# Performance work log

Hardware: AMD Instinct MI355X
Metric: run time of the kernel (lower is better)

## Reference

```python
import jax, jax.numpy as jnp
import numpy as np

B, N, D_IN, D_OUT = 2, 2048, 2048, 2048
H, G = 32, 8            # num_heads, num_kv_groups
HD = D_OUT // H         # head_dim = 64
R = H // G              # group_size = 4


def _rope(x, cos, sin):
    # x: (b, h, n, hd); cos/sin: (n, hd)
    hd = x.shape[-1]
    x1, x2 = x[..., : hd // 2], x[..., hd // 2:]
    rotated = jnp.concatenate((-x2, x1), axis=-1)
    return x * cos[None, None] + rotated * sin[None, None]


def setup_inputs() -> dict:
    key = jax.random.key(0)
    ks = jax.random.split(key, 6)
    x = jax.random.normal(ks[0], (B, N, D_IN), dtype=jnp.float32)
    # standard RoPE tables over full head_dim (rotate-half convention)
    inv_freq = 1.0 / (10000.0 ** (np.arange(0, HD, 2, dtype=np.float32) / HD))
    t = np.arange(N, dtype=np.float32)
    freqs = np.outer(t, inv_freq)                      # (n, hd/2)
    emb = np.concatenate([freqs, freqs], axis=-1)      # (n, hd)
    cos = jnp.asarray(np.cos(emb), dtype=jnp.float32)
    sin = jnp.asarray(np.sin(emb), dtype=jnp.float32)
    mask = jnp.triu(jnp.ones((N, N), dtype=bool), k=1)  # True above diagonal -> masked
    s = 0.02
    Wq = jax.random.normal(ks[1], (D_IN, D_OUT), dtype=jnp.float32) * s
    Wk = jax.random.normal(ks[2], (D_IN, G * HD), dtype=jnp.float32) * s
    Wv = jax.random.normal(ks[3], (D_IN, G * HD), dtype=jnp.float32) * s
    Wo = jax.random.normal(ks[4], (D_OUT, D_OUT), dtype=jnp.float32) * s
    return {"x": x, "cos": cos, "sin": sin, "mask": mask,
            "Wq": Wq, "Wk": Wk, "Wv": Wv, "Wo": Wo}


def reference(x, cos, sin, mask, Wq, Wk, Wv, Wo):
    b, n, _ = x.shape
    q = (x @ Wq).reshape(b, n, H, HD).transpose(0, 2, 1, 3)   # (b, H, n, hd)
    k = (x @ Wk).reshape(b, n, G, HD).transpose(0, 2, 1, 3)   # (b, G, n, hd)
    v = (x @ Wv).reshape(b, n, G, HD).transpose(0, 2, 1, 3)   # (b, G, n, hd)
    q = _rope(q, cos, sin)
    k = _rope(k, cos, sin)
    # grouped attention: avoid physically repeating KV heads
    qg = q.reshape(b, G, R, n, HD)                            # (b, G, r, n, hd)
    scores = jnp.einsum('bgrnd,bgmd->bgrnm', qg, k)           # (b, G, r, n, n)
    scores = jnp.where(mask[None, None, None], -jnp.inf, scores)
    attn = jax.nn.softmax(scores / jnp.sqrt(jnp.float32(HD)), axis=-1)
    ctx = jnp.einsum('bgrnm,bgmd->bgrnd', attn, v)            # (b, G, r, n, hd)
    ctx = ctx.reshape(b, H, n, HD).transpose(0, 2, 1, 3).reshape(b, n, D_OUT)
    return ctx @ Wo
```

## Files before the change

### kernel.cpp

```cpp
#include <hip/hip_runtime.h>
#include <hip/hip_bf16.h>
#include <stdint.h>

#define B_   2
#define N_   2048
#define DIN  2048
#define DOUT 2048
#define H_   32
#define G_   8
#define HD_  64
#define M_   (B_*N_)

using short8 = __attribute__((ext_vector_type(8))) short;
using f32x4  = __attribute__((ext_vector_type(4))) float;
using f32x16 = __attribute__((ext_vector_type(16))) float;
using int4v  = __attribute__((ext_vector_type(4))) int;

__device__ __forceinline__ unsigned short f2bf(float f) {
  unsigned int u = __float_as_uint(f);
  unsigned int r = u + 0x7FFFu + ((u >> 16) & 1u);
  return (unsigned short)(r >> 16);
}
__device__ __forceinline__ float bf2f(unsigned short h) {
  return __uint_as_float(((unsigned int)h) << 16);
}

__global__ void k_cvt(const float* __restrict__ in, unsigned short* __restrict__ out, int n4) {
  int i = blockIdx.x * 256 + threadIdx.x;
  if (i >= n4) return;
  float4 v = reinterpret_cast<const float4*>(in)[i];
  uint2 o;
  o.x = (unsigned int)f2bf(v.x) | ((unsigned int)f2bf(v.y) << 16);
  o.y = (unsigned int)f2bf(v.z) | ((unsigned int)f2bf(v.w) << 16);
  reinterpret_cast<uint2*>(out)[i] = o;
}

__global__ void k_transpose_all(const float* __restrict__ Wq, const float* __restrict__ Wk,
                                const float* __restrict__ Wv, const float* __restrict__ Wo,
                                unsigned short* __restrict__ Wqkv_t,
                                unsigned short* __restrict__ Wo_t) {
  __shared__ float tile[32][33];
  const int ct = blockIdx.x;
  const int r0 = blockIdx.y * 32;
  const float* W;
  unsigned short* dst;
  int C, c0, dstRow;
  if (ct < 64)      { W = Wq; dst = Wqkv_t; C = 2048; c0 = ct*32;      dstRow = c0; }
  else if (ct < 80) { W = Wk; dst = Wqkv_t; C = 512;  c0 = (ct-64)*32; dstRow = 2048 + c0; }
  else if (ct < 96) { W = Wv; dst = Wqkv_t; C = 512;  c0 = (ct-80)*32; dstRow = 2560 + c0; }
  else              { W = Wo; dst = Wo_t;   C = 2048; c0 = (ct-96)*32; dstRow = c0; }
  const int tx = threadIdx.x, ty = threadIdx.y;
  #pragma unroll
  for (int j = 0; j < 4; ++j)
    tile[ty + j*8][tx] = W[(size_t)(r0 + ty + j*8) * C + c0 + tx];
  __syncthreads();
  #pragma unroll
  for (int j = 0; j < 4; ++j)
    dst[(size_t)(dstRow + ty + j*8) * 2048 + r0 + tx] = f2bf(tile[tx][ty + j*8]);
}

#define A0OFF 0
#define B0OFF 32768
#define A1OFF 65536
#define B1OFF 98304

#define QPHASE(ABUF, M0, STAGES, WAITS)                                          \
  {                                                                              \
    short8 a00 = rdA(ABUF, M0, 0),   a01 = rdA(ABUF, M0, 1);                     \
    short8 a10 = rdA(ABUF, M0+1, 0), a11 = rdA(ABUF, M0+1, 1);                   \
    STAGES;                                                                      \
    WAITS;                                                                       \
    __builtin_amdgcn_s_barrier();                                                \
    asm volatile("s_waitcnt lgkmcnt(0)" ::: "memory");                           \
    __builtin_amdgcn_sched_barrier(0);                                           \
    __builtin_amdgcn_s_setprio(1);                                               \
    _Pragma("unroll")                                                            \
    for (int n = 0; n < 4; ++n) {                                                \
      acc[M0][n]   = __builtin_amdgcn_mfma_f32_16x16x32_bf16(a00, bv[n][0], acc[M0][n], 0,0,0);   \
      acc[M0][n]   = __builtin_amdgcn_mfma_f32_16x16x32_bf16(a01, bv[n][1], acc[M0][n], 0,0,0);   \
      acc[M0+1][n] = __builtin_amdgcn_mfma_f32_16x16x32_bf16(a10, bv[n][0], acc[M0+1][n], 0,0,0); \
      acc[M0+1][n] = __builtin_amdgcn_mfma_f32_16x16x32_bf16(a11, bv[n][1], acc[M0+1][n], 0,0,0); \
    }                                                                            \
    __builtin_amdgcn_s_setprio(0);                                               \
    __builtin_amdgcn_s_barrier();                                                \
  }

__global__ void __launch_bounds__(512, 2)
k_gemm_qkv(const unsigned short* __restrict__ A, const unsigned short* __restrict__ Bt,
           unsigned short* __restrict__ Qp, unsigned short* __restrict__ Kp,
           unsigned short* __restrict__ Vp,
           const float* __restrict__ cosT, const float* __restrict__ sinT) {
  __shared__ unsigned short sm[65536];
  const int tid = threadIdx.x;
  const int wid = tid >> 6, l = tid & 63;
  const int lrow = l & 15, lk = l >> 4;
  const int wm = wid >> 2, wn = wid & 3;

  const int gx   = gridDim.x;
  const int nwg  = gx * gridDim.y;
  const int orig = blockIdx.y * gx + blockIdx.x;
  const int q8   = nwg >> 3;
  const int xcd  = orig & 7, lin = orig >> 3;
  const int wg   = xcd * q8 + lin;
  const int bx   = wg % gx, by = wg / gx;
  const int rowA0 = by * 256, rowB0 = bx * 256;

  f32x4 acc[8][4];
  #pragma unroll
  for (int m = 0; m < 8; ++m)
    #pragma unroll
    for (int n = 0; n < 4; ++n)
      #pragma unroll
      for (int r = 0; r < 4; ++r) acc[m][n][r] = 0.f;

  const int srowoff = wid*8 + (l >> 3);
  const int skoff   = (((l & 7) ^ ((l >> 3) & 7)) << 3);
  auto stageHalf = [&](const unsigned short* Mat, int rowBase, int t, int bufByte, int half) {
    #pragma unroll
    for (int j = 0; j < 2; ++j) {
      const unsigned short* g = Mat + (size_t)(rowBase + half*128 + j*64 + srowoff) * 2048
                                    + t*64 + skoff;
      __builtin_amdgcn_global_load_lds(
          (const __attribute__((address_space(1))) unsigned int*)g,
          (__attribute__((address_space(3))) unsigned int*)
              ((char*)sm + bufByte + half*16384 + j*8192 + wid*1024),
          16, 0, 0);
    }
  };

  const int aswz = (lrow & 7) << 4;
  auto rdA = [&](int bufByte, int m, int kk) -> short8 {
    int byte = bufByte + (wm*128 + m*16 + lrow)*128 + ((kk*64 + lk*16) ^ aswz);
    return *reinterpret_cast<const short8*>((char*)sm + byte);
  };
  auto rdB = [&](int bufByte, int n, int kk) -> short8 {
    int byte = bufByte + (wn*64 + n*16 + lrow)*128 + ((kk*64 + lk*16) ^ aswz);
    return *reinterpret_cast<const short8*>((char*)sm + byte);
  };

  short8 bv[4][2];

  stageHalf(Bt, rowB0, 0, B0OFF, 0); stageHalf(Bt, rowB0, 0, B0OFF, 1);
  stageHalf(A,  rowA0, 0, A0OFF, 0); stageHalf(A,  rowA0, 0, A0OFF, 1);
  stageHalf(Bt, rowB0, 1, B1OFF, 0); stageHalf(Bt, rowB0, 1, B1OFF, 1);
  asm volatile("s_waitcnt vmcnt(4)" ::: "memory");
  __builtin_amdgcn_sched_barrier(0);
  __builtin_amdgcn_s_barrier();

  for (int i = 0; i < 16; ++i) {
    const int t = 2*i;
    const bool more = (i < 15);

    #pragma unroll
    for (int n = 0; n < 4; ++n) { bv[n][0] = rdB(B0OFF, n, 0); bv[n][1] = rdB(B0OFF, n, 1); }
    QPHASE(A0OFF, 0, { stageHalf(A, rowA0, t+1, A1OFF, 0);
                       stageHalf(A, rowA0, t+1, A1OFF, 1); }, {});
    QPHASE(A0OFF, 2, { if (more) stageHalf(Bt, rowB0, t+2, B0OFF, 0); }, {});
    QPHASE(A0OFF, 4, { if (more) stageHalf(Bt, rowB0, t+2, B0OFF, 1); }, {});
    QPHASE(A0OFF, 6, {}, { if (more) { asm volatile("s_waitcnt vmcnt(4)" ::: "memory"); }
                           else      { asm volatile("s_waitcnt vmcnt(0)" ::: "memory"); }
                           __builtin_amdgcn_sched_barrier(0); });

    #pragma unroll
    for (int n = 0; n < 4; ++n) { bv[n][0] = rdB(B1OFF, n, 0); bv[n][1] = rdB(B1OFF, n, 1); }
    QPHASE(A1OFF, 0, { if (more) stageHalf(A, rowA0, t+2, A0OFF, 0); }, {});
    QPHASE(A1OFF, 2, { if (more) stageHalf(A, rowA0, t+2, A0OFF, 1); }, {});
    QPHASE(A1OFF, 4, { if (more) stageHalf(Bt, rowB0, t+3, B1OFF, 0); }, {});
    QPHASE(A1OFF, 6, { if (more) { stageHalf(Bt, rowB0, t+3, B1OFF, 1);
                                   asm volatile("s_waitcnt vmcnt(4)" ::: "memory");
                                   __builtin_amdgcn_sched_barrier(0); } }, {});
  }

  if (rowB0 >= 2560) {
    const int bq = rowA0 >> 11;
    #pragma unroll
    for (int m = 0; m < 8; ++m) {
      const int row0 = rowA0 + wm*128 + m*16 + lk*4;
      const int key  = row0 & 2047;
      const size_t tbase = (size_t)(key >> 5)*2048 + (size_t)((key >> 4) & 1)*512
                         + (size_t)((key >> 3) & 1)*256 + (size_t)(key & 7);
      #pragma unroll
      for (int n = 0; n < 4; ++n) {
        const int cv = rowB0 + wn*64 + n*16 + lrow - 2560;
        const int gq = cv >> 6, d = cv & 63;
        const size_t addr = (size_t)(bq*8 + gq)*131072 + tbase
                          + (size_t)(d >> 5)*1024 + (size_t)(d & 31)*8;
        ushort4 st;
        st.x = f2bf(acc[m][n][0]); st.y = f2bf(acc[m][n][1]);
        st.z = f2bf(acc[m][n][2]); st.w = f2bf(acc[m][n][3]);
        *reinterpret_cast<ushort4*>(Vp + addr) = st;
      }
    }
  } else {
    const bool isQ = (rowB0 < 2048);
    const float scale = isQ ? 0.18033688011112042f : 1.0f;
    unsigned short* dst = isQ ? Qp : Kp;
    #pragma unroll
    for (int m = 0; m < 8; ++m) {
      const int row0 = rowA0 + wm*128 + m*16 + lk*4;
      const int b = row0 >> 11;
      #pragma unroll
      for (int n = 0; n < 2; ++n) {
        const int col = rowB0 + wn*64 + n*16 + lrow;
        const int e   = n*16 + lrow;
        const int hg  = isQ ? (col >> 6) : ((col - 2048) >> 6);
        const size_t chunk = (size_t)(isQ ? (b*32 + hg) : (b*8 + hg)) * 64;
        #pragma unroll
        for (int r = 0; r < 4; ++r) {
          const int pos = (row0 + r) & 2047;
          const float cc = cosT[pos*64 + e] * scale;
          const float ss = sinT[pos*64 + e] * scale;
          const float x1 = acc[m][n][r];
          const float x2 = acc[m][n+2][r];
          const size_t off = (chunk + (pos >> 5)) * 2048
                           + (size_t)(e >> 4)*512 + (size_t)((e >> 3) & 1)*256
                           + (size_t)(pos & 31)*8 + (e & 7);
          dst[off]        = f2bf(x1*cc - x2*ss);
          dst[off + 1024] = f2bf(x2*cc + x1*ss);
        }
      }
    }
  }
}

#define OA0 0
#define OB0 32768
#define OA1 49152
#define OB1 81920

#define OPHASE(ABUF, M, STAGES, WAITS)                                           \
  {                                                                              \
    short8 a0 = rdA(ABUF, M, 0), a1 = rdA(ABUF, M, 1);                           \
    STAGES;                                                                      \
    WAITS;                                                                       \
    __builtin_amdgcn_s_barrier();                                                \
    asm volatile("s_waitcnt lgkmcnt(0)" ::: "memory");                           \
    __builtin_amdgcn_sched_barrier(0);                                           \
    __builtin_amdgcn_s_setprio(1);                                               \
    _Pragma("unroll")                                                            \
    for (int n = 0; n < 4; ++n) {                                                \
      acc[M][n] = __builtin_amdgcn_mfma_f32_16x16x32_bf16(a0, bv[n][0], acc[M][n], 0,0,0); \
      acc[M][n] = __builtin_amdgcn_mfma_f32_16x16x32_bf16(a1, bv[n][1], acc[M][n], 0,0,0); \
    }                                                                            \
    __builtin_amdgcn_s_setprio(0);                                               \
    __builtin_amdgcn_s_barrier();                                                \
  }

__global__ void __launch_bounds__(512, 2)
k_gemm_out(const unsigned short* __restrict__ A, const unsigned short* __restrict__ Bt,
           float* __restrict__ C) {
  __shared__ unsigned short sm[49152];
  const int tid = threadIdx.x;
  const int wid = tid >> 6, l = tid & 63;
  const int lrow = l & 15, lk = l >> 4;
  const int wm = wid >> 1, wn = wid & 1;

  const int gx   = gridDim.x;
  const int nwg  = gx * gridDim.y;
  const int orig = blockIdx.y * gx + blockIdx.x;
  const int q8   = nwg >> 3;
  const int xcd  = orig & 7, lin = orig >> 3;
  const int wg   = xcd * q8 + lin;
  const int bx   = wg % gx, by = wg / gx;
  const int rowA0 = by * 256, rowB0 = bx * 128;

  f32x4 acc[4][4];
  #pragma unroll
  for (int m = 0; m < 4; ++m)
    #pragma unroll
    for (int n = 0; n < 4; ++n)
      #pragma unroll
      for (int r = 0; r < 4; ++r) acc[m][n][r] = 0.f;

  const int srowoff = wid*8 + (l >> 3);
  const int skoff   = (((l & 7) ^ ((l >> 3) & 7)) << 3);
  auto stageU = [&](const unsigned short* Mat, int rowBase, int t, int bufByte, int u) {
    const unsigned short* g = Mat + (size_t)(rowBase + u*64 + srowoff) * 2048 + t*64 + skoff;
    __builtin_amdgcn_global_load_lds(
        (const __attribute__((address_space(1))) unsigned int*)g,
        (__attribute__((address_space(3))) unsigned int*)
            ((char*)sm + bufByte + u*8192 + wid*1024),
        16, 0, 0);
  };

  const int aswz = (lrow & 7) << 4;
  auto rdA = [&](int bufByte, int m, int kk) -> short8 {
    int byte = bufByte + (wm*64 + m*16 + lrow)*128 + ((kk*64 + lk*16) ^ aswz);
    return *reinterpret_cast<const short8*>((char*)sm + byte);
  };
  auto rdB = [&](int bufByte, int n, int kk) -> short8 {
    int byte = bufByte + (wn*64 + n*16 + lrow)*128 + ((kk*64 + lk*16) ^ aswz);
    return *reinterpret_cast<const short8*>((char*)sm + byte);
  };

  short8 bv[4][2];

  stageU(Bt, rowB0, 0, OB0, 0); stageU(Bt, rowB0, 0, OB0, 1);
  stageU(A,  rowA0, 0, OA0, 0); stageU(A,  rowA0, 0, OA0, 1);
  stageU(A,  rowA0, 0, OA0, 2); stageU(A,  rowA0, 0, OA0, 3);
  stageU(Bt, rowB0, 1, OB1, 0); stageU(Bt, rowB0, 1, OB1, 1);
  asm volatile("s_waitcnt vmcnt(2)" ::: "memory");
  __builtin_amdgcn_sched_barrier(0);
  __builtin_amdgcn_s_barrier();

  for (int i = 0; i < 16; ++i) {
    const int t = 2*i;
    const bool more = (i < 15);

    #pragma unroll
    for (int n = 0; n < 4; ++n) { bv[n][0] = rdB(OB0, n, 0); bv[n][1] = rdB(OB0, n, 1); }
    OPHASE(OA0, 0, { stageU(A, rowA0, t+1, OA1, 0); stageU(A, rowA0, t+1, OA1, 1); }, {});
    OPHASE(OA0, 1, { stageU(A, rowA0, t+1, OA1, 2); stageU(A, rowA0, t+1, OA1, 3); }, {});
    OPHASE(OA0, 2, { if (more) { stageU(Bt, rowB0, t+2, OB0, 0);
                                 stageU(Bt, rowB0, t+2, OB0, 1); } }, {});
    OPHASE(OA0, 3, {}, { if (more) { asm volatile("s_waitcnt vmcnt(2)" ::: "memory"); }
                         else      { asm volatile("s_waitcnt vmcnt(0)" ::: "memory"); }
                         __builtin_amdgcn_sched_barrier(0); });

    #pragma unroll
    for (int n = 0; n < 4; ++n) { bv[n][0] = rdB(OB1, n, 0); bv[n][1] = rdB(OB1, n, 1); }
    OPHASE(OA1, 0, { if (more) { stageU(A, rowA0, t+2, OA0, 0);
                                 stageU(A, rowA0, t+2, OA0, 1); } }, {});
    OPHASE(OA1, 1, { if (more) { stageU(A, rowA0, t+2, OA0, 2);
                                 stageU(A, rowA0, t+2, OA0, 3); } }, {});
    OPHASE(OA1, 2, { if (more) { stageU(Bt, rowB0, t+3, OB1, 0);
                                 stageU(Bt, rowB0, t+3, OB1, 1); } }, {});
    OPHASE(OA1, 3, {}, { if (more) { asm volatile("s_waitcnt vmcnt(2)" ::: "memory"); }
                         else      { asm volatile("s_waitcnt vmcnt(0)" ::: "memory"); }
                         __builtin_amdgcn_sched_barrier(0); });
  }

  #pragma unroll
  for (int m = 0; m < 4; ++m) {
    int row0 = rowA0 + wm*64 + m*16 + lk*4;
    #pragma unroll
    for (int n = 0; n < 4; ++n) {
      int col = rowB0 + wn*64 + n*16 + lrow;
      #pragma unroll
      for (int r = 0; r < 4; ++r)
        C[(size_t)(row0 + r) * DOUT + col] = acc[m][n][r];
    }
  }
}

__global__ void __launch_bounds__(256, 3)
k_attn(const unsigned short* __restrict__ Qp, const unsigned short* __restrict__ Kp,
       const unsigned short* __restrict__ Vp, unsigned short* __restrict__ ctx) {
  __shared__ unsigned short kvlds[2][4096];
  const int bid = blockIdx.x;
  const int c   = bid & 15;
  const int b   = c >> 3, g = c & 7;
  const int w   = bid >> 4;
  const int jj  = w >> 4, x = w & 15;
  const int qt  = (jj == 0) ? 63 - x : (jj == 1) ? 32 + x : (jj == 2) ? 31 - x : x;
  const int tid = threadIdx.x;
  const int hh  = tid >> 6;
  const int h   = g*4 + hh;
  const int l   = tid & 63;
  const int lq  = l & 31, hi = l >> 5;

  const unsigned short* qbase = Qp + ((size_t)(b*32 + h)*64 + qt)*2048 + l*8;
  short8 qf0 = *reinterpret_cast<const short8*>(qbase);
  short8 qf1 = *reinterpret_cast<const short8*>(qbase + 512);
  short8 qf2 = *reinterpret_cast<const short8*>(qbase + 1024);
  short8 qf3 = *reinterpret_cast<const short8*>(qbase + 1536);

  const unsigned short* ksrc = Kp + (size_t)c*131072 + hh*512 + l*8;
  const unsigned short* vsrc = Vp + (size_t)c*131072 + hh*512 + l*8;

  f32x16 acc0, acc1;
  #pragma unroll
  for (int r = 0; r < 16; ++r) { acc0[r] = 0.f; acc1[r] = 0.f; }
  float l_run = 0.f;

  auto stage = [&](int t, int buf) {
    __builtin_amdgcn_global_load_lds(
        (const __attribute__((address_space(1))) unsigned int*)(ksrc + (size_t)t*2048),
        (__attribute__((address_space(3))) unsigned int*)((char*)&kvlds[buf][0] + hh*1024),
        16, 0, 0);
    __builtin_amdgcn_global_load_lds(
        (const __attribute__((address_space(1))) unsigned int*)(vsrc + (size_t)t*2048),
        (__attribute__((address_space(3))) unsigned int*)((char*)&kvlds[buf][2048] + hh*1024),
        16, 0, 0);
  };

  auto body = [&](bool diag, int buf) {
    short8 ka = *reinterpret_cast<const short8*>(&kvlds[buf][l*8]);
    short8 kb = *reinterpret_cast<const short8*>(&kvlds[buf][512 + l*8]);
    short8 kc = *reinterpret_cast<const short8*>(&kvlds[buf][1024 + l*8]);
    short8 kd = *reinterpret_cast<const short8*>(&kvlds[buf][1536 + l*8]);

    f32x16 s;
    #pragma unroll
    for (int r = 0; r < 16; ++r) s[r] = 0.f;
    __builtin_amdgcn_s_setprio(1);
    s = __builtin_amdgcn_mfma_f32_32x32x16_bf16(ka, qf0, s, 0, 0, 0);
    s = __builtin_amdgcn_mfma_f32_32x32x16_bf16(kb, qf1, s, 0, 0, 0);
    s = __builtin_amdgcn_mfma_f32_32x32x16_bf16(kc, qf2, s, 0, 0, 0);
    s = __builtin_amdgcn_mfma_f32_32x32x16_bf16(kd, qf3, s, 0, 0, 0);
    __builtin_amdgcn_s_setprio(0);

    if (diag) {
      #pragma unroll
      for (int r = 0; r < 16; ++r) {
        const int ko = (r & 3) + 8*(r >> 2) + 4*hi;
        s[r] = (ko <= lq) ? s[r] : -3.0e38f;
      }
    }

    unsigned int w8[8];
    float ps = 0.f;
    #pragma unroll
    for (int i = 0; i < 8; ++i) {
      float p0 = exp2f(s[2*i]);
      float p1 = exp2f(s[2*i+1]);
      ps += p0 + p1;
      asm("v_cvt_pk_bf16_f32 %0, %1, %2" : "=v"(w8[i]) : "v"(p0), "v"(p1));
    }
    ps += __shfl_xor(ps, 32);
    l_run += ps;

    unsigned int x0 = w8[0], x1 = w8[1], y0 = w8[2], y1 = w8[3];
    asm("v_permlane32_swap_b32 %0, %1" : "+v"(x0), "+v"(y0));
    asm("v_permlane32_swap_b32 %0, %1" : "+v"(x1), "+v"(y1));
    unsigned int x2 = w8[4], x3 = w8[5], y2 = w8[6], y3 = w8[7];
    asm("v_permlane32_swap_b32 %0, %1" : "+v"(x2), "+v"(y2));
    asm("v_permlane32_swap_b32 %0, %1" : "+v"(x3), "+v"(y3));
    int4v p0i, p1i;
    p0i[0] = (int)x0; p0i[1] = (int)x1; p0i[2] = (int)y0; p0i[3] = (int)y1;
    p1i[0] = (int)x2; p1i[1] = (int)x3; p1i[2] = (int)y2; p1i[3] = (int)y3;
    short8 pa0 = __builtin_bit_cast(short8, p0i);
    short8 pa1 = __builtin_bit_cast(short8, p1i);

    short8 va = *reinterpret_cast<const short8*>(&kvlds[buf][2048 + l*8]);
    short8 vb = *reinterpret_cast<const short8*>(&kvlds[buf][2560 + l*8]);
    short8 vc = *reinterpret_cast<const short8*>(&kvlds[buf][3072 + l*8]);
    short8 vd = *reinterpret_cast<const short8*>(&kvlds[buf][3584 + l*8]);

    __builtin_amdgcn_s_setprio(1);
    acc0 = __builtin_amdgcn_mfma_f32_32x32x16_bf16(va, pa0, acc0, 0, 0, 0);
    acc0 = __builtin_amdgcn_mfma_f32_32x32x16_bf16(vb, pa1, acc0, 0, 0, 0);
    acc1 = __builtin_amdgcn_mfma_f32_32x32x16_bf16(vc, pa0, acc1, 0, 0, 0);
    acc1 = __builtin_amdgcn_mfma_f32_32x32x16_bf16(vd, pa1, acc1, 0, 0, 0);
    __builtin_amdgcn_s_setprio(0);
  };

  stage(0, 0);
  __syncthreads();
  for (int t = 0; ; ) {
    const int cur = t & 1;
    if (t < qt) stage(t + 1, cur ^ 1);
    body(t == qt, cur);
    if (++t > qt) break;
    __syncthreads();
  }

  const float rl = 1.f / l_run;
  unsigned short* op = ctx + (size_t)(b*N_ + qt*32 + lq) * DOUT + h*HD_ + 4*hi;
  #pragma unroll
  for (int dt = 0; dt < 2; ++dt) {
    #pragma unroll
    for (int rq = 0; rq < 4; ++rq) {
      const float a0 = (dt ? acc1[4*rq+0] : acc0[4*rq+0]) * rl;
      const float a1 = (dt ? acc1[4*rq+1] : acc0[4*rq+1]) * rl;
      const float a2 = (dt ? acc1[4*rq+2] : acc0[4*rq+2]) * rl;
      const float a3 = (dt ? acc1[4*rq+3] : acc0[4*rq+3]) * rl;
      ushort4 st;
      st.x = f2bf(a0); st.y = f2bf(a1); st.z = f2bf(a2); st.w = f2bf(a3);
      *reinterpret_cast<ushort4*>(op + dt*32 + rq*8) = st;
    }
  }
}

extern "C" void kernel_launch(void* const* d_in, const int* in_sizes, int n_in,
                              void* d_out, int out_size, void* d_ws, size_t ws_size,
                              hipStream_t stream) {
  const float* x    = (const float*)d_in[0];
  const float* cosT = (const float*)d_in[1];
  const float* sinT = (const float*)d_in[2];
  const float* Wq   = (const float*)d_in[4];
  const float* Wk   = (const float*)d_in[5];
  const float* Wv   = (const float*)d_in[6];
  const float* Wo   = (const float*)d_in[7];
  float* out = (float*)d_out;

  char* ws = (char*)d_ws;
  unsigned short* xb     = (unsigned short*)(ws);
  unsigned short* ctxb   = xb;
  unsigned short* Wqkv_t = (unsigned short*)(ws + 16777216);
  unsigned short* Wo_t   = (unsigned short*)(ws + 29360128);
  unsigned short* Qp     = (unsigned short*)(ws + 37748736);
  unsigned short* Kp     = (unsigned short*)(ws + 54525952);
  unsigned short* Vp     = (unsigned short*)(ws + 58720256);

  k_cvt<<<dim3(M_*DIN/4/256), dim3(256), 0, stream>>>(x, xb, M_*DIN/4);

  k_transpose_all<<<dim3(160, 64), dim3(32, 8), 0, stream>>>(
      Wq, Wk, Wv, Wo, Wqkv_t, Wo_t);

  k_gemm_qkv<<<dim3(3072/256, M_/256), 512, 0, stream>>>(
      xb, Wqkv_t, Qp, Kp, Vp, cosT, sinT);

  k_attn<<<dim3(1024), dim3(256), 0, stream>>>(Qp, Kp, Vp, ctxb);

  k_gemm_out<<<dim3(DOUT/128, M_/256), 512, 0, stream>>>(ctxb, Wo_t, out);
}
```

Before: 173.5 us.

## Retile QKV GEMM to 256x192 with permuted RoPE columns and fuse prep kernels

The QKV projection GEMM changes from 256x256 tiles to 256x192 tiles with a 4x2 wave layout, which gives 16x16=256 workgroups instead of 12x16=192 and fills the GPU better. The Q/K weight columns are permuted during the transpose so that each wave's 32-column pair holds matching RoPE halves, letting the epilogue rotate within one j-group across the mixed Q/K/V tile boundaries. The x conversion and weight transpose are merged into one k_prep launch to save a kernel launch. The trade-off is a smaller N-tile and less reuse of A per workgroup, plus a more complex per-column epilogue branch.

New measurement: 166.3 us. 4.1% less time.

```diff
diff --git a/kernel.cpp b/kernel.cpp
--- a/kernel.cpp
+++ b/kernel.cpp
@@ -25,49 +25,54 @@
   return __uint_as_float(((unsigned int)h) << 16);
 }
 
-__global__ void k_cvt(const float* __restrict__ in, unsigned short* __restrict__ out, int n4) {
-  int i = blockIdx.x * 256 + threadIdx.x;
-  if (i >= n4) return;
-  float4 v = reinterpret_cast<const float4*>(in)[i];
-  uint2 o;
-  o.x = (unsigned int)f2bf(v.x) | ((unsigned int)f2bf(v.y) << 16);
-  o.y = (unsigned int)f2bf(v.z) | ((unsigned int)f2bf(v.w) << 16);
-  reinterpret_cast<uint2*>(out)[i] = o;
-}
-
-__global__ void k_transpose_all(const float* __restrict__ Wq, const float* __restrict__ Wk,
-                                const float* __restrict__ Wv, const float* __restrict__ Wo,
-                                unsigned short* __restrict__ Wqkv_t,
-                                unsigned short* __restrict__ Wo_t) {
+__device__ __forceinline__ int p63(int e) {
+  return (((e >> 4) ^ (e >> 5)) & 1) ? (e ^ 48) : e;
+}
+
+__global__ void k_prep(const float* __restrict__ x, unsigned short* __restrict__ xb,
+                       const float* __restrict__ Wq, const float* __restrict__ Wk,
+                       const float* __restrict__ Wv, const float* __restrict__ Wo,
+                       unsigned short* __restrict__ Wqkv_t, unsigned short* __restrict__ Wo_t) {
   __shared__ float tile[32][33];
   const int ct = blockIdx.x;
+  const int tx = threadIdx.x, ty = threadIdx.y;
+  if (ct >= 160) {
+    const int i = ((ct - 160) * 64 + blockIdx.y) * 256 + ty * 32 + tx;
+    float4 v = reinterpret_cast<const float4*>(x)[i];
+    uint2 o;
+    o.x = (unsigned int)f2bf(v.x) | ((unsigned int)f2bf(v.y) << 16);
+    o.y = (unsigned int)f2bf(v.z) | ((unsigned int)f2bf(v.w) << 16);
+    reinterpret_cast<uint2*>(xb)[i] = o;
+    return;
+  }
   const int r0 = blockIdx.y * 32;
   const float* W;
   unsigned short* dst;
-  int C, c0, dstRow;
-  if (ct < 64)      { W = Wq; dst = Wqkv_t; C = 2048; c0 = ct*32;      dstRow = c0; }
-  else if (ct < 80) { W = Wk; dst = Wqkv_t; C = 512;  c0 = (ct-64)*32; dstRow = 2048 + c0; }
-  else if (ct < 96) { W = Wv; dst = Wqkv_t; C = 512;  c0 = (ct-80)*32; dstRow = 2560 + c0; }
-  else              { W = Wo; dst = Wo_t;   C = 2048; c0 = (ct-96)*32; dstRow = c0; }
-  const int tx = threadIdx.x, ty = threadIdx.y;
+  int C, c0, base, rope;
+  if (ct < 64)      { W = Wq; dst = Wqkv_t; C = 2048; c0 = ct*32;      base = 0;    rope = 1; }
+  else if (ct < 80) { W = Wk; dst = Wqkv_t; C = 512;  c0 = (ct-64)*32; base = 2048; rope = 1; }
+  else if (ct < 96) { W = Wv; dst = Wqkv_t; C = 512;  c0 = (ct-80)*32; base = 2560; rope = 0; }
+  else              { W = Wo; dst = Wo_t;   C = 2048; c0 = (ct-96)*32; base = 0;    rope = 0; }
   #pragma unroll
   for (int j = 0; j < 4; ++j)
     tile[ty + j*8][tx] = W[(size_t)(r0 + ty + j*8) * C + c0 + tx];
   __syncthreads();
   #pragma unroll
-  for (int j = 0; j < 4; ++j)
-    dst[(size_t)(dstRow + ty + j*8) * 2048 + r0 + tx] = f2bf(tile[tx][ty + j*8]);
-}
-
-#define A0OFF 0
-#define B0OFF 32768
-#define A1OFF 65536
-#define B1OFF 98304
-
-#define QPHASE(ABUF, M0, STAGES, WAITS)                                          \
+  for (int j = 0; j < 4; ++j) {
+    int colW = c0 + ty + j*8;
+    int row  = rope ? ((colW & ~63) | p63(colW & 63)) : colW;
+    dst[(size_t)(base + row) * 2048 + r0 + tx] = f2bf(tile[tx][ty + j*8]);
+  }
+}
+
+#define QA0 0
+#define QB0 32768
+#define QA1 57344
+#define QB1 90112
+
+#define QP3(ABUF, M, STAGES, WAITS)                                              \
   {                                                                              \
-    short8 a00 = rdA(ABUF, M0, 0),   a01 = rdA(ABUF, M0, 1);                     \
-    short8 a10 = rdA(ABUF, M0+1, 0), a11 = rdA(ABUF, M0+1, 1);                   \
+    short8 a0 = rdA(ABUF, M, 0), a1 = rdA(ABUF, M, 1);                           \
     STAGES;                                                                      \
     WAITS;                                                                       \
     __builtin_amdgcn_s_barrier();                                                \
@@ -75,11 +80,9 @@
     __builtin_amdgcn_sched_barrier(0);                                           \
     __builtin_amdgcn_s_setprio(1);                                               \
     _Pragma("unroll")                                                            \
-    for (int n = 0; n < 4; ++n) {                                                \
-      acc[M0][n]   = __builtin_amdgcn_mfma_f32_16x16x32_bf16(a00, bv[n][0], acc[M0][n], 0,0,0);   \
-      acc[M0][n]   = __builtin_amdgcn_mfma_f32_16x16x32_bf16(a01, bv[n][1], acc[M0][n], 0,0,0);   \
-      acc[M0+1][n] = __builtin_amdgcn_mfma_f32_16x16x32_bf16(a10, bv[n][0], acc[M0+1][n], 0,0,0); \
-      acc[M0+1][n] = __builtin_amdgcn_mfma_f32_16x16x32_bf16(a11, bv[n][1], acc[M0+1][n], 0,0,0); \
+    for (int n = 0; n < 6; ++n) {                                                \
+      acc[M][n] = __builtin_amdgcn_mfma_f32_16x16x32_bf16(a0, bv[n][0], acc[M][n], 0,0,0); \
+      acc[M][n] = __builtin_amdgcn_mfma_f32_16x16x32_bf16(a1, bv[n][1], acc[M][n], 0,0,0); \
     }                                                                            \
     __builtin_amdgcn_s_setprio(0);                                               \
     __builtin_amdgcn_s_barrier();                                                \
@@ -90,11 +93,11 @@
            unsigned short* __restrict__ Qp, unsigned short* __restrict__ Kp,
            unsigned short* __restrict__ Vp,
            const float* __restrict__ cosT, const float* __restrict__ sinT) {
-  __shared__ unsigned short sm[65536];
+  __shared__ unsigned short sm[57344];
   const int tid = threadIdx.x;
   const int wid = tid >> 6, l = tid & 63;
   const int lrow = l & 15, lk = l >> 4;
-  const int wm = wid >> 2, wn = wid & 3;
+  const int wm = wid >> 1, wn = wid & 1;
 
   const int gx   = gridDim.x;
   const int nwg  = gx * gridDim.y;
@@ -103,47 +106,44 @@
   const int xcd  = orig & 7, lin = orig >> 3;
   const int wg   = xcd * q8 + lin;
   const int bx   = wg % gx, by = wg / gx;
-  const int rowA0 = by * 256, rowB0 = bx * 256;
-
-  f32x4 acc[8][4];
-  #pragma unroll
-  for (int m = 0; m < 8; ++m)
-    #pragma unroll
-    for (int n = 0; n < 4; ++n)
+  const int rowA0 = by * 256, rowB0 = bx * 192;
+
+  f32x4 acc[4][6];
+  #pragma unroll
+  for (int m = 0; m < 4; ++m)
+    #pragma unroll
+    for (int n = 0; n < 6; ++n)
       #pragma unroll
       for (int r = 0; r < 4; ++r) acc[m][n][r] = 0.f;
 
   const int srowoff = wid*8 + (l >> 3);
   const int skoff   = (((l & 7) ^ ((l >> 3) & 7)) << 3);
-  auto stageHalf = [&](const unsigned short* Mat, int rowBase, int t, int bufByte, int half) {
-    #pragma unroll
-    for (int j = 0; j < 2; ++j) {
-      const unsigned short* g = Mat + (size_t)(rowBase + half*128 + j*64 + srowoff) * 2048
-                                    + t*64 + skoff;
-      __builtin_amdgcn_global_load_lds(
-          (const __attribute__((address_space(1))) unsigned int*)g,
-          (__attribute__((address_space(3))) unsigned int*)
-              ((char*)sm + bufByte + half*16384 + j*8192 + wid*1024),
-          16, 0, 0);
-    }
+  auto stageU = [&](const unsigned short* Mat, int rowBase, int t, int bufByte, int u) {
+    const unsigned short* g = Mat + (size_t)(rowBase + u*64 + srowoff) * 2048 + t*64 + skoff;
+    __builtin_amdgcn_global_load_lds(
+        (const __attribute__((address_space(1))) unsigned int*)g,
+        (__attribute__((address_space(3))) unsigned int*)
+            ((char*)sm + bufByte + u*8192 + wid*1024),
+        16, 0, 0);
   };
 
   const int aswz = (lrow & 7) << 4;
   auto rdA = [&](int bufByte, int m, int kk) -> short8 {
-    int byte = bufByte + (wm*128 + m*16 + lrow)*128 + ((kk*64 + lk*16) ^ aswz);
+    int byte = bufByte + (wm*64 + m*16 + lrow)*128 + ((kk*64 + lk*16) ^ aswz);
     return *reinterpret_cast<const short8*>((char*)sm + byte);
   };
   auto rdB = [&](int bufByte, int n, int kk) -> short8 {
-    int byte = bufByte + (wn*64 + n*16 + lrow)*128 + ((kk*64 + lk*16) ^ aswz);
+    int byte = bufByte + (wn*96 + n*16 + lrow)*128 + ((kk*64 + lk*16) ^ aswz);
     return *reinterpret_cast<const short8*>((char*)sm + byte);
   };
 
-  short8 bv[4][2];
-
-  stageHalf(Bt, rowB0, 0, B0OFF, 0); stageHalf(Bt, rowB0, 0, B0OFF, 1);
-  stageHalf(A,  rowA0, 0, A0OFF, 0); stageHalf(A,  rowA0, 0, A0OFF, 1);
-  stageHalf(Bt, rowB0, 1, B1OFF, 0); stageHalf(Bt, rowB0, 1, B1OFF, 1);
-  asm volatile("s_waitcnt vmcnt(4)" ::: "memory");
+  short8 bv[6][2];
+
+  stageU(Bt, rowB0, 0, QB0, 0); stageU(Bt, rowB0, 0, QB0, 1); stageU(Bt, rowB0, 0, QB0, 2);
+  stageU(A,  rowA0, 0, QA0, 0); stageU(A,  rowA0, 0, QA0, 1);
+  stageU(A,  rowA0, 0, QA0, 2); stageU(A,  rowA0, 0, QA0, 3);
+  stageU(Bt, rowB0, 1, QB1, 0); stageU(Bt, rowB0, 1, QB1, 1); stageU(Bt, rowB0, 1, QB1, 2);
+  asm volatile("s_waitcnt vmcnt(3)" ::: "memory");
   __builtin_amdgcn_sched_barrier(0);
   __builtin_amdgcn_s_barrier();
 
@@ -152,66 +152,67 @@
     const bool more = (i < 15);
 
     #pragma unroll
-    for (int n = 0; n < 4; ++n) { bv[n][0] = rdB(B0OFF, n, 0); bv[n][1] = rdB(B0OFF, n, 1); }
-    QPHASE(A0OFF, 0, { stageHalf(A, rowA0, t+1, A1OFF, 0);
-                       stageHalf(A, rowA0, t+1, A1OFF, 1); }, {});
-    QPHASE(A0OFF, 2, { if (more) stageHalf(Bt, rowB0, t+2, B0OFF, 0); }, {});
-    QPHASE(A0OFF, 4, { if (more) stageHalf(Bt, rowB0, t+2, B0OFF, 1); }, {});
-    QPHASE(A0OFF, 6, {}, { if (more) { asm volatile("s_waitcnt vmcnt(4)" ::: "memory"); }
-                           else      { asm volatile("s_waitcnt vmcnt(0)" ::: "memory"); }
-                           __builtin_amdgcn_sched_barrier(0); });
-
-    #pragma unroll
-    for (int n = 0; n < 4; ++n) { bv[n][0] = rdB(B1OFF, n, 0); bv[n][1] = rdB(B1OFF, n, 1); }
-    QPHASE(A1OFF, 0, { if (more) stageHalf(A, rowA0, t+2, A0OFF, 0); }, {});
-    QPHASE(A1OFF, 2, { if (more) stageHalf(A, rowA0, t+2, A0OFF, 1); }, {});
-    QPHASE(A1OFF, 4, { if (more) stageHalf(Bt, rowB0, t+3, B1OFF, 0); }, {});
-    QPHASE(A1OFF, 6, { if (more) { stageHalf(Bt, rowB0, t+3, B1OFF, 1);
-                                   asm volatile("s_waitcnt vmcnt(4)" ::: "memory");
-                                   __builtin_amdgcn_sched_barrier(0); } }, {});
-  }
-
-  if (rowB0 >= 2560) {
-    const int bq = rowA0 >> 11;
-    #pragma unroll
-    for (int m = 0; m < 8; ++m) {
-      const int row0 = rowA0 + wm*128 + m*16 + lk*4;
-      const int key  = row0 & 2047;
-      const size_t tbase = (size_t)(key >> 5)*2048 + (size_t)((key >> 4) & 1)*512
-                         + (size_t)((key >> 3) & 1)*256 + (size_t)(key & 7);
-      #pragma unroll
-      for (int n = 0; n < 4; ++n) {
-        const int cv = rowB0 + wn*64 + n*16 + lrow - 2560;
-        const int gq = cv >> 6, d = cv & 63;
-        const size_t addr = (size_t)(bq*8 + gq)*131072 + tbase
-                          + (size_t)(d >> 5)*1024 + (size_t)(d & 31)*8;
-        ushort4 st;
-        st.x = f2bf(acc[m][n][0]); st.y = f2bf(acc[m][n][1]);
-        st.z = f2bf(acc[m][n][2]); st.w = f2bf(acc[m][n][3]);
-        *reinterpret_cast<ushort4*>(Vp + addr) = st;
-      }
-    }
-  } else {
-    const bool isQ = (rowB0 < 2048);
-    const float scale = isQ ? 0.18033688011112042f : 1.0f;
-    unsigned short* dst = isQ ? Qp : Kp;
-    #pragma unroll
-    for (int m = 0; m < 8; ++m) {
-      const int row0 = rowA0 + wm*128 + m*16 + lk*4;
-      const int b = row0 >> 11;
-      #pragma unroll
-      for (int n = 0; n < 2; ++n) {
-        const int col = rowB0 + wn*64 + n*16 + lrow;
-        const int e   = n*16 + lrow;
-        const int hg  = isQ ? (col >> 6) : ((col - 2048) >> 6);
+    for (int n = 0; n < 6; ++n) { bv[n][0] = rdB(QB0, n, 0); bv[n][1] = rdB(QB0, n, 1); }
+    QP3(QA0, 0, { stageU(A, rowA0, t+1, QA1, 0); stageU(A, rowA0, t+1, QA1, 1); }, {});
+    QP3(QA0, 1, { stageU(A, rowA0, t+1, QA1, 2); stageU(A, rowA0, t+1, QA1, 3); }, {});
+    QP3(QA0, 2, { if (more) { stageU(Bt, rowB0, t+2, QB0, 0);
+                              stageU(Bt, rowB0, t+2, QB0, 1); } }, {});
+    QP3(QA0, 3, { if (more) stageU(Bt, rowB0, t+2, QB0, 2); },
+                { if (more) { asm volatile("s_waitcnt vmcnt(3)" ::: "memory"); }
+                  else      { asm volatile("s_waitcnt vmcnt(0)" ::: "memory"); }
+                  __builtin_amdgcn_sched_barrier(0); });
+
+    #pragma unroll
+    for (int n = 0; n < 6; ++n) { bv[n][0] = rdB(QB1, n, 0); bv[n][1] = rdB(QB1, n, 1); }
+    QP3(QA1, 0, { if (more) { stageU(A, rowA0, t+2, QA0, 0);
+                              stageU(A, rowA0, t+2, QA0, 1); } }, {});
+    QP3(QA1, 1, { if (more) { stageU(A, rowA0, t+2, QA0, 2);
+                              stageU(A, rowA0, t+2, QA0, 3); } }, {});
+    QP3(QA1, 2, { if (more) { stageU(Bt, rowB0, t+3, QB1, 0);
+                              stageU(Bt, rowB0, t+3, QB1, 1); } }, {});
+    QP3(QA1, 3, { if (more) stageU(Bt, rowB0, t+3, QB1, 2); },
+                { if (more) { asm volatile("s_waitcnt vmcnt(3)" ::: "memory"); }
+                  else      { asm volatile("s_waitcnt vmcnt(0)" ::: "memory"); }
+                  __builtin_amdgcn_sched_barrier(0); });
+  }
+
+  #pragma unroll
+  for (int m = 0; m < 4; ++m) {
+    const int row0 = rowA0 + wm*64 + m*16 + lk*4;
+    const int b    = row0 >> 11;
+    const int key  = row0 & 2047;
+    #pragma unroll
+    for (int j = 0; j < 3; ++j) {
+      const int col0 = rowB0 + wn*96 + j*32 + lrow;
+      if (col0 >= 2560) {
+        const size_t tbase = (size_t)(key >> 5)*2048 + (size_t)((key >> 4) & 1)*512
+                           + (size_t)((key >> 3) & 1)*256 + (size_t)(key & 7);
+        #pragma unroll
+        for (int f = 0; f < 2; ++f) {
+          const int cv = col0 + f*16 - 2560;
+          const int gq = cv >> 6, d = cv & 63;
+          const size_t addr = (size_t)(b*8 + gq)*131072 + tbase
+                            + (size_t)(d >> 5)*1024 + (size_t)(d & 31)*8;
+          ushort4 st;
+          st.x = f2bf(acc[m][2*j+f][0]); st.y = f2bf(acc[m][2*j+f][1]);
+          st.z = f2bf(acc[m][2*j+f][2]); st.w = f2bf(acc[m][2*j+f][3]);
+          *reinterpret_cast<ushort4*>(Vp + addr) = st;
+        }
+      } else {
+        const bool isQ = (col0 < 2048);
+        const float scale = isQ ? 0.18033688011112042f : 1.0f;
+        unsigned short* dst = isQ ? Qp : Kp;
+        const int ch = col0 & 63;
+        const int e  = ch - ((ch & 32) ? 16 : 0);
+        const int hg = isQ ? (col0 >> 6) : ((col0 - 2048) >> 6);
         const size_t chunk = (size_t)(isQ ? (b*32 + hg) : (b*8 + hg)) * 64;
         #pragma unroll
         for (int r = 0; r < 4; ++r) {
-          const int pos = (row0 + r) & 2047;
+          const int pos = key + r;
           const float cc = cosT[pos*64 + e] * scale;
           const float ss = sinT[pos*64 + e] * scale;
-          const float x1 = acc[m][n][r];
-          const float x2 = acc[m][n+2][r];
+          const float x1 = acc[m][2*j][r];
+          const float x2 = acc[m][2*j+1][r];
           const size_t off = (chunk + (pos >> 5)) * 2048
                            + (size_t)(e >> 4)*512 + (size_t)((e >> 3) & 1)*256
                            + (size_t)(pos & 31)*8 + (e & 7);
@@ -493,12 +494,10 @@
   unsigned short* Kp     = (unsigned short*)(ws + 54525952);
   unsigned short* Vp     = (unsigned short*)(ws + 58720256);
 
-  k_cvt<<<dim3(M_*DIN/4/256), dim3(256), 0, stream>>>(x, xb, M_*DIN/4);
-
-  k_transpose_all<<<dim3(160, 64), dim3(32, 8), 0, stream>>>(
-      Wq, Wk, Wv, Wo, Wqkv_t, Wo_t);
-
-  k_gemm_qkv<<<dim3(3072/256, M_/256), 512, 0, stream>>>(
+  k_prep<<<dim3(288, 64), dim3(32, 8), 0, stream>>>(
+      x, xb, Wq, Wk, Wv, Wo, Wqkv_t, Wo_t);
+
+  k_gemm_qkv<<<dim3(3072/192, M_/256), 512, 0, stream>>>(
       xb, Wqkv_t, Qp, Kp, Vp, cosT, sinT);
 
   k_attn<<<dim3(1024), dim3(256), 0, stream>>>(Qp, Kp, Vp, ctxb);
```
